# Kernel tuning notes

Measured on AMD Instinct MI355X. Metric: run time of the kernel, lower is better.

## Reference

```python
import jax, jax.numpy as jnp
import numpy as np
from jax import lax

B, T, C_IN, HID, K, HORIZON = 64, 1024, 256, 512, 3, 12
OUT_DIM = HORIZON * 3


def causal_conv(x, w, b, dilation):
    # x: (B, C_in, T), w: (C_out, C_in, K) -> left-padded causal conv == conv+Chomp1d
    pad = (K - 1) * dilation
    y = lax.conv_general_dilated(x, w, window_strides=(1,), padding=[(pad, 0)],
                                 rhs_dilation=(dilation,),
                                 dimension_numbers=('NCH', 'OIH', 'NCH'))
    return y + b[None, :, None]


def setup_inputs() -> dict:
    key = jax.random.key(0)
    ks = jax.random.split(key, 16)
    N = B * T
    x = jax.random.normal(ks[0], (N, C_IN), jnp.float32)
    edge_index = jax.random.randint(ks[1], (2, N), 0, N, dtype=jnp.int64)
    idx = jnp.arange(N, dtype=jnp.int64)
    batch = idx // T          # graph id per node
    node_time = idx % T       # local time per node
    s1 = 1.0 / np.sqrt(C_IN * K)
    s2 = 1.0 / np.sqrt(HID * K)
    sd = 1.0 / np.sqrt(C_IN)
    sf = 1.0 / np.sqrt(HID)
    return {
        'x': x, 'edge_index': edge_index, 'batch': batch, 'node_time': node_time,
        # TemporalBlock 0 (in=C_IN, out=HID, dilation=1)
        'conv1_w0': jax.random.uniform(ks[2], (HID, C_IN, K), jnp.float32, -s1, s1),
        'conv1_b0': jax.random.uniform(ks[3], (HID,), jnp.float32, -s1, s1),
        'conv2_w0': jax.random.uniform(ks[4], (HID, HID, K), jnp.float32, -s2, s2),
        'conv2_b0': jax.random.uniform(ks[5], (HID,), jnp.float32, -s2, s2),
        'down_w0': jax.random.uniform(ks[6], (HID, C_IN, 1), jnp.float32, -sd, sd),
        'down_b0': jax.random.uniform(ks[7], (HID,), jnp.float32, -sd, sd),
        # TemporalBlock 1 (in=HID, out=HID, dilation=2, no downsample)
        'conv1_w1': jax.random.uniform(ks[8], (HID, HID, K), jnp.float32, -s2, s2),
        'conv1_b1': jax.random.uniform(ks[9], (HID,), jnp.float32, -s2, s2),
        'conv2_w1': jax.random.uniform(ks[10], (HID, HID, K), jnp.float32, -s2, s2),
        'conv2_b1': jax.random.uniform(ks[11], (HID,), jnp.float32, -s2, s2),
        # fc
        'fc_w': jax.random.uniform(ks[12], (OUT_DIM, HID), jnp.float32, -sf, sf),
        'fc_b': jax.random.uniform(ks[13], (OUT_DIM,), jnp.float32, -sf, sf),
    }


def reference(x, edge_index, batch, node_time,
              conv1_w0, conv1_b0, conv2_w0, conv2_b0, down_w0, down_b0,
              conv1_w1, conv1_b1, conv2_w1, conv2_b1, fc_w, fc_b):
    # vectorized scatter replacing the per-node Python loop
    x_seq = jnp.zeros((B, T, C_IN), x.dtype).at[batch, node_time].set(x)
    h = x_seq.transpose(0, 2, 1)  # (B, C_IN, T)
    # TemporalBlock 0 (dropout inactive in eval)
    out = jax.nn.relu(causal_conv(h, conv1_w0, conv1_b0, 1))
    out = jax.nn.relu(causal_conv(out, conv2_w0, conv2_b0, 1))
    res = jnp.einsum('bct,oc->bot', h, down_w0[:, :, 0]) + down_b0[None, :, None]
    h = jax.nn.relu(out + res)
    # TemporalBlock 1
    out = jax.nn.relu(causal_conv(h, conv1_w1, conv1_b1, 2))
    out = jax.nn.relu(causal_conv(out, conv2_w1, conv2_b1, 2))
    h = jax.nn.relu(out + h)
    # last timestep -> fc
    return h[:, :, -1] @ fc_w.T + fc_b
```

## Files before the change

kernel.cpp:

```cpp
#include <hip/hip_runtime.h>


#define OUTD 36

template <int CIN, int TS_N, int TP, int TOUT, int S, int D, int OFF, int TAPS,
          int OCT, int CCH, int NCH, bool SRC_X, int TS_BASE, int TS_STEP>
__global__ __launch_bounds__(256) void k_conv(const float* __restrict__ src,
                                              const float* __restrict__ w,
                                              float* __restrict__ Pout) {
    const int tid = threadIdx.x, lane = tid & 63, wv = tid >> 6;
    const int oc0 = blockIdx.x * OCT;
    constexpr int OCR = OCT / 4;
    __shared__ float Als[CCH * TAPS * OCT];
    __shared__ float Bls[CCH * 64 * TP];
    float acc[OCR][TOUT];
#pragma unroll
    for (int i = 0; i < OCR; ++i)
#pragma unroll
        for (int t = 0; t < TOUT; ++t) acc[i][t] = 0.f;

    for (int ch = 0; ch < NCH; ++ch) {
        const int c0 = (blockIdx.y * NCH + ch) * CCH;
        if (ch) __syncthreads();
        for (int idx = tid; idx < OCT * CCH * TAPS; idx += 256) {
            int i = idx / (CCH * TAPS), r = idx % (CCH * TAPS);
            int c = r / TAPS, kk = r % TAPS;
            Als[(c * TAPS + kk) * OCT + i] =
                w[(size_t)(oc0 + i) * (CIN * TAPS) + (c0 + c) * TAPS + kk];
        }
        if constexpr (SRC_X) {
            for (int idx = tid; idx < CCH * TS_N * 64; idx += 256) {
                int c = idx % CCH, rb = idx / CCH;
                int b = rb & 63, u = rb >> 6;
                Bls[(c * 64 + b) * TP + u] =
                    src[((size_t)b * 1024 + 1011 + TS_BASE + TS_STEP * u) * 256 +
                        c0 + c];
            }
        } else {
            const float4* gp = (const float4*)(src + (size_t)c0 * 64 * TP);
            float4* lp = (float4*)Bls;
            for (int idx = tid; idx < CCH * 64 * TP / 4; idx += 256)
                lp[idx] = gp[idx];
        }
        __syncthreads();
        constexpr int NLOAD = (TP % 4 == 0) ? TP : TS_N;
        for (int c = 0; c < CCH; ++c) {
            float bv[NLOAD];
            if constexpr (TP % 4 == 0) {
#pragma unroll
                for (int q = 0; q < TP / 4; ++q)
                    *(float4*)&bv[4 * q] =
                        *(const float4*)&Bls[(c * 64 + lane) * TP + 4 * q];
            } else {
#pragma unroll
                for (int u = 0; u < TS_N; ++u)
                    bv[u] = Bls[(c * 64 + lane) * TP + u];
            }
            float av[TAPS][OCR];
#pragma unroll
            for (int kk = 0; kk < TAPS; ++kk)
#pragma unroll
                for (int j = 0; j < OCR; j += 4)
                    *(float4*)&av[kk][j] =
                        *(const float4*)&Als[(c * TAPS + kk) * OCT + wv * OCR + j];
#pragma unroll
            for (int i = 0; i < OCR; ++i)
#pragma unroll
                for (int t = 0; t < TOUT; ++t)
#pragma unroll
                    for (int kk = 0; kk < TAPS; ++kk)
                        acc[i][t] += av[kk][i] * bv[S * t + D * kk + OFF];
        }
    }
#pragma unroll
    for (int i = 0; i < OCR; ++i)
#pragma unroll
        for (int t = 0; t < TOUT; ++t)
            Pout[(((size_t)blockIdx.y * 512 + oc0 + wv * OCR + i) * TOUT + t) * 64 +
                 lane] = acc[i][t];
}

template <int KS1, int T, int TPo, int KS2, bool RES>
__global__ __launch_bounds__(256) void k_red(const float* __restrict__ P1,
                                             const float* __restrict__ bias1,
                                             const float* __restrict__ P2,
                                             const float* __restrict__ bias2,
                                             const float* __restrict__ res,
                                             float* __restrict__ outp) {
    const int oc = blockIdx.x, tid = threadIdx.x;
    __shared__ float Sm[64 * TPo];
    if constexpr (TPo > 1) {
        for (int i = tid; i < 64 * TPo; i += 256) Sm[i] = 0.f;
        __syncthreads();
    }
    if (tid < T * 16) {
        const int t = tid / 16, b4 = (tid % 16) * 4;
        float4 s = make_float4(0.f, 0.f, 0.f, 0.f);
#pragma unroll
        for (int p = 0; p < KS1; ++p) {
            float4 u =
                *(const float4*)(P1 + (((size_t)p * 512 + oc) * T + t) * 64 + b4);
            s.x += u.x; s.y += u.y; s.z += u.z; s.w += u.w;
        }
        const float b1 = bias1[oc];
        s.x = fmaxf(s.x + b1, 0.f); s.y = fmaxf(s.y + b1, 0.f);
        s.z = fmaxf(s.z + b1, 0.f); s.w = fmaxf(s.w + b1, 0.f);
        if constexpr (KS2 > 0) {
            float4 s2 = make_float4(0.f, 0.f, 0.f, 0.f);
#pragma unroll
            for (int p = 0; p < KS2; ++p) {
                float4 u =
                    *(const float4*)(P2 + (((size_t)p * 512 + oc) * T + t) * 64 + b4);
                s2.x += u.x; s2.y += u.y; s2.z += u.z; s2.w += u.w;
            }
            const float b2v = bias2[oc];
            s.x = fmaxf(s.x + s2.x + b2v, 0.f);
            s.y = fmaxf(s.y + s2.y + b2v, 0.f);
            s.z = fmaxf(s.z + s2.z + b2v, 0.f);
            s.w = fmaxf(s.w + s2.w + b2v, 0.f);
        }
        if constexpr (RES) {
            s.x = fmaxf(s.x + res[((size_t)oc * 64 + b4 + 0) * 12 + 4], 0.f);
            s.y = fmaxf(s.y + res[((size_t)oc * 64 + b4 + 1) * 12 + 4], 0.f);
            s.z = fmaxf(s.z + res[((size_t)oc * 64 + b4 + 2) * 12 + 4], 0.f);
            s.w = fmaxf(s.w + res[((size_t)oc * 64 + b4 + 3) * 12 + 4], 0.f);
        }
        if constexpr (TPo == 1) {
            *(float4*)(outp + (size_t)oc * 64 + b4) = s;
        } else {
            Sm[(b4 + 0) * TPo + t] = s.x;
            Sm[(b4 + 1) * TPo + t] = s.y;
            Sm[(b4 + 2) * TPo + t] = s.z;
            Sm[(b4 + 3) * TPo + t] = s.w;
        }
    }
    if constexpr (TPo > 1) {
        __syncthreads();
        float4* op = (float4*)(outp + (size_t)oc * 64 * TPo);
        for (int i = tid; i < 64 * TPo / 4; i += 256)
            op[i] = *(const float4*)&Sm[4 * i];
    }
}

__global__ __launch_bounds__(64) void k_fc(const float* __restrict__ H1,
                                           const float* __restrict__ fcw,
                                           const float* __restrict__ fcb,
                                           float* __restrict__ out) {
    const int j = blockIdx.x, lane = threadIdx.x;
    float acc = fcb[j];
#pragma unroll 8
    for (int o = 0; o < 512; ++o) acc += fcw[j * 512 + o] * H1[o * 64 + lane];
    out[lane * OUTD + j] = acc;
}

extern "C" void kernel_launch(void* const* d_in, const int* in_sizes, int n_in,
                              void* d_out, int out_size, void* d_ws, size_t ws_size,
                              hipStream_t stream) {
    const float* x    = (const float*)d_in[0];
    const float* w1_0 = (const float*)d_in[4];
    const float* b1_0 = (const float*)d_in[5];
    const float* w2_0 = (const float*)d_in[6];
    const float* b2_0 = (const float*)d_in[7];
    const float* wd0  = (const float*)d_in[8];
    const float* bd0  = (const float*)d_in[9];
    const float* w1_1 = (const float*)d_in[10];
    const float* b1_1 = (const float*)d_in[11];
    const float* w2_1 = (const float*)d_in[12];
    const float* b2_1 = (const float*)d_in[13];
    const float* fcw  = (const float*)d_in[14];
    const float* fcb  = (const float*)d_in[15];
    float* out = (float*)d_out;

    float* P0  = (float*)d_ws;
    float* B1  = P0 + 8 * 512 * 11 * 64;
    float* P1  = B1 + 512 * 64 * 12;
    float* PD  = P1 + 16 * 512 * 5 * 64;
    float* H0  = PD + 8 * 512 * 5 * 64;
    float* P2  = H0 + 512 * 64 * 12;
    float* B2  = P2 + 16 * 512 * 3 * 64;
    float* P3  = B2 + 512 * 64 * 4;
    float* H1g = P3 + 8 * 512 * 64;

    k_conv<256, 13, 13, 11, 1, 1, 0, 3, 16, 16, 2, true, 0, 1>
        <<<dim3(32, 8), 256, 0, stream>>>(x, w1_0, P0);
    k_conv<256, 5, 5, 5, 1, 0, 0, 1, 32, 16, 2, true, 4, 2>
        <<<dim3(16, 8), 256, 0, stream>>>(x, wd0, PD);
    k_red<8, 11, 12, 0, false><<<512, 256, 0, stream>>>(P0, b1_0, nullptr,
                                                        nullptr, nullptr, B1);
    k_conv<512, 11, 12, 5, 2, 1, 0, 3, 32, 16, 2, false, 0, 0>
        <<<dim3(16, 16), 256, 0, stream>>>(B1, w2_0, P1);
    k_red<16, 5, 12, 8, false><<<512, 256, 0, stream>>>(P1, b2_0, PD, bd0,
                                                        nullptr, H0);
    k_conv<512, 5, 12, 3, 1, 1, 0, 3, 32, 16, 2, false, 0, 0>
        <<<dim3(16, 16), 256, 0, stream>>>(H0, w1_1, P2);
    k_red<16, 3, 4, 0, false><<<512, 256, 0, stream>>>(P2, b1_1, nullptr,
                                                       nullptr, nullptr, B2);
    k_conv<512, 3, 4, 1, 1, 1, 0, 3, 32, 32, 2, false, 0, 0>
        <<<dim3(16, 8), 256, 0, stream>>>(B2, w2_1, P3);
    k_red<8, 1, 1, 0, true><<<512, 256, 0, stream>>>(P3, b2_1, nullptr, nullptr,
                                                     H0, H1g);
    k_fc<<<OUTD, 64, 0, stream>>>(H1g, fcw, fcb, out);
}
```

Before: 125.0 us.

## Fuse split-K reductions into conv kernels with in-block two-way channel split

Replaces the split-K conv kernels plus separate reduction kernels with four fused conv kernels. Each block splits input channels across two halves, combines the partial sums in shared memory, and applies bias, ReLU and residual in its epilogue. The 1x1 downsample conv is merged into the first kernel's launch. This cuts the launch count from ten to five and removes the partial-sum buffers, at the cost of lower per-thread register blocking (one output channel per thread) and an extra in-block reduction.

```diff
diff --git a/kernel.cpp b/kernel.cpp
--- a/kernel.cpp
+++ b/kernel.cpp
@@ -3,201 +3,186 @@
 
 #define OUTD 36
 
-template <int CIN, int TS_N, int TP, int TOUT, int S, int D, int OFF, int TAPS,
-          int OCT, int CCH, int NCH, bool SRC_X, int TS_BASE, int TS_STEP>
-__global__ __launch_bounds__(256) void k_conv(const float* __restrict__ src,
-                                              const float* __restrict__ w,
-                                              float* __restrict__ Pout) {
-    const int tid = threadIdx.x, lane = tid & 63, wv = tid >> 6;
-    const int oc0 = blockIdx.x * OCT;
-    constexpr int OCR = OCT / 4;
-    __shared__ float Als[CCH * TAPS * OCT];
-    __shared__ float Bls[CCH * 64 * TP];
-    float acc[OCR][TOUT];
+template <int CIN, int TIN, int TOUT, int S, int DD, int TAPS,
+          bool SRC_X, int XBASE, int XSTEP, int SRCPITCH,
+          int EPI, int RESPITCH, int RESBASE, int RESSTEP, int OUTPITCH>
+__device__ __forceinline__ void convfk(
+    int ocp, int bq, const float* __restrict__ src, const float* __restrict__ w,
+    const float* __restrict__ bias, const float* __restrict__ res,
+    float* __restrict__ out, float* smem) {
+  const int tid = threadIdx.x;
+  const int lb = tid & 15, s = tid >> 4, oc_l = s & 7, ch = s >> 3;
+  const int oc = ocp * 8 + oc_l;
+  constexpr int CHALF = CIN / 2;
+  constexpr int NCH = CHALF / 16;
+  constexpr int XSZ = TIN * 16 * 17;
+  constexpr int BSZ = 16 * TIN * 16;
+  constexpr int WSZ = 16 * TAPS * 8;
+  constexpr int ASZ = SRC_X ? XSZ : BSZ;
+  float* Wl = smem + 2 * ASZ;
+  float* Rl = Wl + 2 * WSZ;
+
+  float acc[TOUT];
 #pragma unroll
-    for (int i = 0; i < OCR; ++i)
+  for (int t = 0; t < TOUT; ++t) acc[t] = 0.f;
+
+  for (int i = 0; i < NCH; ++i) {
+    if (i) __syncthreads();
+    if constexpr (SRC_X) {
+      for (int idx = tid; idx < 2 * 16 * TIN * 16; idx += 256) {
+        int h = idx / (16 * TIN * 16), r = idx % (16 * TIN * 16);
+        int c = r & 15, b = (r >> 4) & 15, u = r >> 8;
+        smem[h * XSZ + (u * 16 + b) * 17 + c] =
+            src[((size_t)(bq * 16 + b) * 1024 + 1011 + XBASE + XSTEP * u) * 256 +
+                h * CHALF + i * 16 + c];
+      }
+    } else {
+      for (int idx = tid; idx < 2 * 16 * TIN * 16; idx += 256) {
+        int h = idx / (16 * TIN * 16), r = idx % (16 * TIN * 16);
+        int b = r & 15, u = (r >> 4) % TIN, c = r / (16 * TIN);
+        smem[h * BSZ + (c * TIN + u) * 16 + b] =
+            src[(size_t)(h * CHALF + i * 16 + c) * SRCPITCH + u * 64 +
+                bq * 16 + b];
+      }
+    }
+    for (int idx = tid; idx < 2 * 16 * TAPS * 8; idx += 256) {
+      int s8 = idx & 7, kk = (idx >> 3) % TAPS;
+      int c = (idx / (8 * TAPS)) & 15, h = idx / (8 * TAPS * 16);
+      Wl[h * WSZ + (c * TAPS + kk) * 8 + s8] =
+          w[(size_t)(ocp * 8 + s8) * (CIN * TAPS) +
+            (h * CHALF + i * 16 + c) * TAPS + kk];
+    }
+    __syncthreads();
+    for (int c = 0; c < 16; ++c) {
+      float bv[TIN];
 #pragma unroll
-        for (int t = 0; t < TOUT; ++t) acc[i][t] = 0.f;
-
-    for (int ch = 0; ch < NCH; ++ch) {
-        const int c0 = (blockIdx.y * NCH + ch) * CCH;
-        if (ch) __syncthreads();
-        for (int idx = tid; idx < OCT * CCH * TAPS; idx += 256) {
-            int i = idx / (CCH * TAPS), r = idx % (CCH * TAPS);
-            int c = r / TAPS, kk = r % TAPS;
-            Als[(c * TAPS + kk) * OCT + i] =
-                w[(size_t)(oc0 + i) * (CIN * TAPS) + (c0 + c) * TAPS + kk];
-        }
-        if constexpr (SRC_X) {
-            for (int idx = tid; idx < CCH * TS_N * 64; idx += 256) {
-                int c = idx % CCH, rb = idx / CCH;
-                int b = rb & 63, u = rb >> 6;
-                Bls[(c * 64 + b) * TP + u] =
-                    src[((size_t)b * 1024 + 1011 + TS_BASE + TS_STEP * u) * 256 +
-                        c0 + c];
-            }
-        } else {
-            const float4* gp = (const float4*)(src + (size_t)c0 * 64 * TP);
-            float4* lp = (float4*)Bls;
-            for (int idx = tid; idx < CCH * 64 * TP / 4; idx += 256)
-                lp[idx] = gp[idx];
-        }
-        __syncthreads();
-        constexpr int NLOAD = (TP % 4 == 0) ? TP : TS_N;
-        for (int c = 0; c < CCH; ++c) {
-            float bv[NLOAD];
-            if constexpr (TP % 4 == 0) {
+      for (int u = 0; u < TIN; ++u) {
+        if constexpr (SRC_X)
+          bv[u] = smem[ch * XSZ + (u * 16 + lb) * 17 + c];
+        else
+          bv[u] = smem[ch * BSZ + (c * TIN + u) * 16 + lb];
+      }
+      float wq[TAPS];
 #pragma unroll
-                for (int q = 0; q < TP / 4; ++q)
-                    *(float4*)&bv[4 * q] =
-                        *(const float4*)&Bls[(c * 64 + lane) * TP + 4 * q];
-            } else {
+      for (int kk = 0; kk < TAPS; ++kk)
+        wq[kk] = Wl[ch * WSZ + (c * TAPS + kk) * 8 + oc_l];
 #pragma unroll
-                for (int u = 0; u < TS_N; ++u)
-                    bv[u] = Bls[(c * 64 + lane) * TP + u];
-            }
-            float av[TAPS][OCR];
+      for (int t = 0; t < TOUT; ++t)
 #pragma unroll
-            for (int kk = 0; kk < TAPS; ++kk)
+        for (int kk = 0; kk < TAPS; ++kk)
+          acc[t] += wq[kk] * bv[S * t + DD * kk];
+    }
+  }
+  if (ch == 1) {
 #pragma unroll
-                for (int j = 0; j < OCR; j += 4)
-                    *(float4*)&av[kk][j] =
-                        *(const float4*)&Als[(c * TAPS + kk) * OCT + wv * OCR + j];
+    for (int t = 0; t < TOUT; ++t) Rl[(oc_l * TOUT + t) * 16 + lb] = acc[t];
+  }
+  __syncthreads();
+  if (ch == 0) {
+    const float bb = bias[oc];
 #pragma unroll
-            for (int i = 0; i < OCR; ++i)
-#pragma unroll
-                for (int t = 0; t < TOUT; ++t)
-#pragma unroll
-                    for (int kk = 0; kk < TAPS; ++kk)
-                        acc[i][t] += av[kk][i] * bv[S * t + D * kk + OFF];
-        }
+    for (int t = 0; t < TOUT; ++t) {
+      float v = acc[t] + Rl[(oc_l * TOUT + t) * 16 + lb];
+      if constexpr (EPI == 0) {
+        v = fmaxf(v + bb, 0.f);
+      } else if constexpr (EPI == 1) {
+        v = v + bb;
+      } else {
+        v = fmaxf(v + bb, 0.f);
+        v += res[(size_t)oc * RESPITCH + RESBASE + t * RESSTEP + bq * 16 + lb];
+        v = fmaxf(v, 0.f);
+      }
+      out[(size_t)oc * OUTPITCH + t * 64 + bq * 16 + lb] = v;
     }
-#pragma unroll
-    for (int i = 0; i < OCR; ++i)
-#pragma unroll
-        for (int t = 0; t < TOUT; ++t)
-            Pout[(((size_t)blockIdx.y * 512 + oc0 + wv * OCR + i) * TOUT + t) * 64 +
-                 lane] = acc[i][t];
+  }
 }
 
-template <int KS1, int T, int TPo, int KS2, bool RES>
-__global__ __launch_bounds__(256) void k_red(const float* __restrict__ P1,
-                                             const float* __restrict__ bias1,
-                                             const float* __restrict__ P2,
-                                             const float* __restrict__ bias2,
-                                             const float* __restrict__ res,
-                                             float* __restrict__ outp) {
-    const int oc = blockIdx.x, tid = threadIdx.x;
-    __shared__ float Sm[64 * TPo];
-    if constexpr (TPo > 1) {
-        for (int i = tid; i < 64 * TPo; i += 256) Sm[i] = 0.f;
-        __syncthreads();
-    }
-    if (tid < T * 16) {
-        const int t = tid / 16, b4 = (tid % 16) * 4;
-        float4 s = make_float4(0.f, 0.f, 0.f, 0.f);
-#pragma unroll
-        for (int p = 0; p < KS1; ++p) {
-            float4 u =
-                *(const float4*)(P1 + (((size_t)p * 512 + oc) * T + t) * 64 + b4);
-            s.x += u.x; s.y += u.y; s.z += u.z; s.w += u.w;
-        }
-        const float b1 = bias1[oc];
-        s.x = fmaxf(s.x + b1, 0.f); s.y = fmaxf(s.y + b1, 0.f);
-        s.z = fmaxf(s.z + b1, 0.f); s.w = fmaxf(s.w + b1, 0.f);
-        if constexpr (KS2 > 0) {
-            float4 s2 = make_float4(0.f, 0.f, 0.f, 0.f);
-#pragma unroll
-            for (int p = 0; p < KS2; ++p) {
-                float4 u =
-                    *(const float4*)(P2 + (((size_t)p * 512 + oc) * T + t) * 64 + b4);
-                s2.x += u.x; s2.y += u.y; s2.z += u.z; s2.w += u.w;
-            }
-            const float b2v = bias2[oc];
-            s.x = fmaxf(s.x + s2.x + b2v, 0.f);
-            s.y = fmaxf(s.y + s2.y + b2v, 0.f);
-            s.z = fmaxf(s.z + s2.z + b2v, 0.f);
-            s.w = fmaxf(s.w + s2.w + b2v, 0.f);
-        }
-        if constexpr (RES) {
-            s.x = fmaxf(s.x + res[((size_t)oc * 64 + b4 + 0) * 12 + 4], 0.f);
-            s.y = fmaxf(s.y + res[((size_t)oc * 64 + b4 + 1) * 12 + 4], 0.f);
-            s.z = fmaxf(s.z + res[((size_t)oc * 64 + b4 + 2) * 12 + 4], 0.f);
-            s.w = fmaxf(s.w + res[((size_t)oc * 64 + b4 + 3) * 12 + 4], 0.f);
-        }
-        if constexpr (TPo == 1) {
-            *(float4*)(outp + (size_t)oc * 64 + b4) = s;
-        } else {
-            Sm[(b4 + 0) * TPo + t] = s.x;
-            Sm[(b4 + 1) * TPo + t] = s.y;
-            Sm[(b4 + 2) * TPo + t] = s.z;
-            Sm[(b4 + 3) * TPo + t] = s.w;
-        }
-    }
-    if constexpr (TPo > 1) {
-        __syncthreads();
-        float4* op = (float4*)(outp + (size_t)oc * 64 * TPo);
-        for (int i = tid; i < 64 * TPo / 4; i += 256)
-            op[i] = *(const float4*)&Sm[4 * i];
-    }
+__global__ __launch_bounds__(256) void k1(const float* __restrict__ x,
+                                          const float* __restrict__ w1_0,
+                                          const float* __restrict__ b1_0,
+                                          const float* __restrict__ wd0,
+                                          const float* __restrict__ bd0,
+                                          float* __restrict__ B1,
+                                          float* __restrict__ PDs) {
+  __shared__ float smem[9248];
+  const int bid = blockIdx.x;
+  if (bid < 256) {
+    convfk<256, 13, 11, 1, 1, 3, true, 0, 1, 0, 0, 0, 0, 0, 704>(
+        bid >> 2, bid & 3, x, w1_0, b1_0, nullptr, B1, smem);
+  } else {
+    const int q = bid - 256;
+    convfk<256, 5, 5, 1, 0, 1, true, 4, 2, 0, 1, 0, 0, 0, 320>(
+        q >> 2, q & 3, x, wd0, bd0, nullptr, PDs, smem);
+  }
+}
+
+__global__ __launch_bounds__(256) void k2(const float* __restrict__ B1,
+                                          const float* __restrict__ w2_0,
+                                          const float* __restrict__ b2_0,
+                                          const float* __restrict__ PDs,
+                                          float* __restrict__ H0) {
+  __shared__ float smem[7040];
+  convfk<512, 11, 5, 2, 1, 3, false, 0, 0, 704, 2, 320, 0, 64, 320>(
+      blockIdx.x >> 2, blockIdx.x & 3, B1, w2_0, b2_0, PDs, H0, smem);
+}
+
+__global__ __launch_bounds__(256) void k3(const float* __restrict__ H0,
+                                          const float* __restrict__ w1_1,
+                                          const float* __restrict__ b1_1,
+                                          float* __restrict__ B2) {
+  __shared__ float smem[3712];
+  convfk<512, 5, 3, 1, 1, 3, false, 0, 0, 320, 0, 0, 0, 0, 192>(
+      blockIdx.x >> 2, blockIdx.x & 3, H0, w1_1, b1_1, nullptr, B2, smem);
+}
+
+__global__ __launch_bounds__(256) void k4(const float* __restrict__ B2,
+                                          const float* __restrict__ w2_1,
+                                          const float* __restrict__ b2_1,
+                                          const float* __restrict__ H0,
+                                          float* __restrict__ H1) {
+  __shared__ float smem[2432];
+  convfk<512, 3, 1, 1, 1, 3, false, 0, 0, 192, 2, 320, 256, 0, 64>(
+      blockIdx.x >> 2, blockIdx.x & 3, B2, w2_1, b2_1, H0, H1, smem);
 }
 
 __global__ __launch_bounds__(64) void k_fc(const float* __restrict__ H1,
                                            const float* __restrict__ fcw,
                                            const float* __restrict__ fcb,
                                            float* __restrict__ out) {
-    const int j = blockIdx.x, lane = threadIdx.x;
-    float acc = fcb[j];
+  const int j = blockIdx.x, lane = threadIdx.x;
+  float acc = fcb[j];
 #pragma unroll 8
-    for (int o = 0; o < 512; ++o) acc += fcw[j * 512 + o] * H1[o * 64 + lane];
-    out[lane * OUTD + j] = acc;
+  for (int o = 0; o < 512; ++o) acc += fcw[j * 512 + o] * H1[o * 64 + lane];
+  out[lane * OUTD + j] = acc;
 }
 
 extern "C" void kernel_launch(void* const* d_in, const int* in_sizes, int n_in,
                               void* d_out, int out_size, void* d_ws, size_t ws_size,
                               hipStream_t stream) {
-    const float* x    = (const float*)d_in[0];
-    const float* w1_0 = (const float*)d_in[4];
-    const float* b1_0 = (const float*)d_in[5];
-    const float* w2_0 = (const float*)d_in[6];
-    const float* b2_0 = (const float*)d_in[7];
-    const float* wd0  = (const float*)d_in[8];
-    const float* bd0  = (const float*)d_in[9];
-    const float* w1_1 = (const float*)d_in[10];
-    const float* b1_1 = (const float*)d_in[11];
-    const float* w2_1 = (const float*)d_in[12];
-    const float* b2_1 = (const float*)d_in[13];
-    const float* fcw  = (const float*)d_in[14];
-    const float* fcb  = (const float*)d_in[15];
-    float* out = (float*)d_out;
+  const float* x    = (const float*)d_in[0];
+  const float* w1_0 = (const float*)d_in[4];
+  const float* b1_0 = (const float*)d_in[5];
+  const float* w2_0 = (const float*)d_in[6];
+  const float* b2_0 = (const float*)d_in[7];
+  const float* wd0  = (const float*)d_in[8];
+  const float* bd0  = (const float*)d_in[9];
+  const float* w1_1 = (const float*)d_in[10];
+  const float* b1_1 = (const float*)d_in[11];
+  const float* w2_1 = (const float*)d_in[12];
+  const float* b2_1 = (const float*)d_in[13];
+  const float* fcw  = (const float*)d_in[14];
+  const float* fcb  = (const float*)d_in[15];
+  float* out = (float*)d_out;
 
-    float* P0  = (float*)d_ws;
-    float* B1  = P0 + 8 * 512 * 11 * 64;
-    float* P1  = B1 + 512 * 64 * 12;
-    float* PD  = P1 + 16 * 512 * 5 * 64;
-    float* H0  = PD + 8 * 512 * 5 * 64;
-    float* P2  = H0 + 512 * 64 * 12;
-    float* B2  = P2 + 16 * 512 * 3 * 64;
-    float* P3  = B2 + 512 * 64 * 4;
-    float* H1g = P3 + 8 * 512 * 64;
+  float* B1  = (float*)d_ws;
+  float* PDs = B1 + 360448;
+  float* H0  = PDs + 163840;
+  float* B2  = H0 + 163840;
+  float* H1  = B2 + 98304;
 
-    k_conv<256, 13, 13, 11, 1, 1, 0, 3, 16, 16, 2, true, 0, 1>
-        <<<dim3(32, 8), 256, 0, stream>>>(x, w1_0, P0);
-    k_conv<256, 5, 5, 5, 1, 0, 0, 1, 32, 16, 2, true, 4, 2>
-        <<<dim3(16, 8), 256, 0, stream>>>(x, wd0, PD);
-    k_red<8, 11, 12, 0, false><<<512, 256, 0, stream>>>(P0, b1_0, nullptr,
-                                                        nullptr, nullptr, B1);
-    k_conv<512, 11, 12, 5, 2, 1, 0, 3, 32, 16, 2, false, 0, 0>
-        <<<dim3(16, 16), 256, 0, stream>>>(B1, w2_0, P1);
-    k_red<16, 5, 12, 8, false><<<512, 256, 0, stream>>>(P1, b2_0, PD, bd0,
-                                                        nullptr, H0);
-    k_conv<512, 5, 12, 3, 1, 1, 0, 3, 32, 16, 2, false, 0, 0>
-        <<<dim3(16, 16), 256, 0, stream>>>(H0, w1_1, P2);
-    k_red<16, 3, 4, 0, false><<<512, 256, 0, stream>>>(P2, b1_1, nullptr,
-                                                       nullptr, nullptr, B2);
-    k_conv<512, 3, 4, 1, 1, 1, 0, 3, 32, 32, 2, false, 0, 0>
-        <<<dim3(16, 8), 256, 0, stream>>>(B2, w2_1, P3);
-    k_red<8, 1, 1, 0, true><<<512, 256, 0, stream>>>(P3, b2_1, nullptr, nullptr,
-                                                     H0, H1g);
-    k_fc<<<OUTD, 64, 0, stream>>>(H1g, fcw, fcb, out);
+  k1<<<512, 256, 0, stream>>>(x, w1_0, b1_0, wd0, bd0, B1, PDs);
+  k2<<<256, 256, 0, stream>>>(B1, w2_0, b2_0, PDs, H0);
+  k3<<<256, 256, 0, stream>>>(H0, w1_1, b1_1, B2);
+  k4<<<256, 256, 0, stream>>>(B2, w2_1, b2_1, H0, H1);
+  k_fc<<<OUTD, 64, 0, stream>>>(H1, fcw, fcb, out);
 }
```

After: 274.8 us. 120% more time.
